# Kernel optimization log

Measured on AMD Instinct MI355X. Metric: run time of the kernel, lower is better.

Reference implementation:

```python
import jax, jax.numpy as jnp
import numpy as np

B, L, DQ, DK, NH = 32, 2048, 1024, 1024, 16
DH = DK // NH  # per-head dim = 64

def setup_inputs() -> dict:
    key = jax.random.key(0)
    ks = jax.random.split(key, 8)
    sq = np.sqrt(2.0 / (DQ + DH)).astype(np.float32)
    sk = np.sqrt(2.0 / (DK + DH)).astype(np.float32)
    return {
        "q": jax.random.normal(ks[0], (B, DQ), jnp.float32),
        "k": jax.random.normal(ks[1], (B, L, DK), jnp.float32),
        "Wq": jax.random.normal(ks[2], (NH * DH, DQ), jnp.float32) * sq,
        "bq": jnp.zeros((NH * DH,), jnp.float32),
        "Wk": jax.random.normal(ks[3], (NH * DH, DK), jnp.float32) * sk,
        "bk": jnp.zeros((NH * DH,), jnp.float32),
        "Wv": jax.random.normal(ks[4], (NH * DH, DK), jnp.float32) * sk,
        "bv": jnp.zeros((NH * DH,), jnp.float32),
    }

def reference(q, k, Wq, bq, Wk, bk, Wv, bv):
    # projections (standard GEMMs), reshape to heads
    qs = (q @ Wq.T + bq).reshape(B, NH, DH)            # [b,n,dh]
    ksr = (k @ Wk.T + bk).reshape(B, L, NH, DH)        # [b,l,n,dh]
    vs = (k @ Wv.T + bv).reshape(B, L, NH, DH)         # [b,l,n,dh]
    temp = jnp.sqrt(jnp.asarray(DH, qs.dtype))
    # single-query attention scores per head, softmax over l
    attn = jnp.einsum('bnd,blnd->bnl', qs, ksr) / temp  # [b,n,l]
    attn = jax.nn.softmax(attn, axis=-1)
    out = jnp.einsum('bnl,blnd->bnd', attn, vs).reshape(B, NH * DH)
    # original returns attn flattened as (n_head*b, l) with head-major order
    attn_flat = jnp.transpose(attn, (1, 0, 2)).reshape(NH * B, L)
    return out, attn_flat
```

## Files before the change

### kernel.cpp

```cpp
#include <hip/hip_runtime.h>
#include <hip/hip_bf16.h>

#define NB 32
#define NL 2048
#define ND 1024
#define NHH 16
#define NDH 64

typedef __bf16 bf16;
typedef __attribute__((ext_vector_type(4))) __bf16 bf16x4;
typedef __attribute__((ext_vector_type(8))) __bf16 bf16x8;
typedef __attribute__((ext_vector_type(4))) float f32x4;

#define SBAR __builtin_amdgcn_s_barrier()
#define WAIT_LGKM0 asm volatile("s_waitcnt lgkmcnt(0)" ::: "memory")
#define WAIT_VM0 asm volatile("s_waitcnt vmcnt(0)" ::: "memory")

#define SWZ(r) (((r) & 7) << 4)

__device__ __forceinline__ float dot4(float4 a, float4 b) {
  return a.x * b.x + a.y * b.y + a.z * b.z + a.w * b.w;
}

__global__ __launch_bounds__(256) void qs_kernel(
    const float* __restrict__ q, const float* __restrict__ Wq,
    const float* __restrict__ bq, float* __restrict__ qs) {
  int o = blockIdx.x;
  int lane = threadIdx.x & 63;
  int wv = threadIdx.x >> 6;
  const float4* wrow = reinterpret_cast<const float4*>(Wq + (size_t)o * ND) + lane * 4;
  float4 w0 = wrow[0], w1 = wrow[1], w2 = wrow[2], w3 = wrow[3];
#pragma unroll
  for (int bb = 0; bb < 8; ++bb) {
    int b = wv * 8 + bb;
    const float4* qr = reinterpret_cast<const float4*>(q + (size_t)b * ND) + lane * 4;
    float s = dot4(qr[0], w0) + dot4(qr[1], w1) + dot4(qr[2], w2) + dot4(qr[3], w3);
#pragma unroll
    for (int off = 32; off > 0; off >>= 1) s += __shfl_down(s, off, 64);
    if (lane == 0) qs[(size_t)b * ND + o] = s + bq[o];
  }
}

__global__ __launch_bounds__(256) void qt_kernel(
    const float* __restrict__ Wk, const float* __restrict__ qs,
    float* __restrict__ qt, const float* __restrict__ bk,
    float* __restrict__ qb) {
  if (blockIdx.x >= 256) {
    int t = (blockIdx.x - 256) * 256 + threadIdx.x;
    if (t < 512) {
      int b = t >> 4, n = t & 15;
      float s = 0.f;
      for (int d = 0; d < 64; ++d)
        s += qs[(size_t)b * ND + n * NDH + d] * bk[n * NDH + d];
      qb[t] = s;
    }
    return;
  }
  int n  = blockIdx.x >> 4;
  int ic = (blockIdx.x >> 2) & 3;
  int bg = blockIdx.x & 3;
  int i = ic * 256 + threadIdx.x;
  __shared__ float s_qs[8][64];
  for (int t = threadIdx.x; t < 512; t += 256) {
    int b = t >> 6, d = t & 63;
    s_qs[b][d] = qs[(size_t)(bg * 8 + b) * ND + n * NDH + d];
  }
  __syncthreads();
  float acc[8];
#pragma unroll
  for (int b = 0; b < 8; ++b) acc[b] = 0.f;
  for (int d = 0; d < 64; ++d) {
    float w = Wk[((size_t)(n * NDH + d)) * ND + i];
#pragma unroll
    for (int b = 0; b < 8; ++b) acc[b] += w * s_qs[b][d];
  }
#pragma unroll
  for (int b = 0; b < 8; ++b)
    qt[((size_t)((bg * 8 + b) * NHH + n)) * ND + i] = acc[b];
}

__global__ __launch_bounds__(512, 4) void fused_kernel(
    const float* __restrict__ kin, const float* __restrict__ qt,
    const float* __restrict__ qb, float* __restrict__ attn,
    float* __restrict__ ctxp) {
  int bx = blockIdx.x;
  int b  = bx >> 3;
  int sl = bx & 7;
  int tid = threadIdx.x, lane = tid & 63, wv = tid >> 6;
  int kg = lane >> 4, ln16 = lane & 15;

  __shared__ __align__(16) float kbf[4][8][1024];
  __shared__ __align__(16) float pbuf[2][8][8][20];
  __shared__ __align__(16) float sP[2][8][20];
  __shared__ __align__(16) float abuf[32][8][16];

  bf16x8 afrag[4];
  {
    const float* qrow = qt + ((size_t)(b * NHH + ln16)) * ND + wv * 128 + kg * 8;
#pragma unroll
    for (int mm = 0; mm < 4; ++mm) {
      f32x4 f0 = *reinterpret_cast<const f32x4*>(qrow + mm * 32);
      f32x4 f1 = *reinterpret_cast<const f32x4*>(qrow + mm * 32 + 4);
      bf16x8 v;
      v[0] = (bf16)f0[0]; v[1] = (bf16)f0[1]; v[2] = (bf16)f0[2]; v[3] = (bf16)f0[3];
      v[4] = (bf16)f1[0]; v[5] = (bf16)f1[1]; v[6] = (bf16)f1[2]; v[7] = (bf16)f1[3];
      afrag[mm] = v;
    }
  }

  int rl = tid & 7, rn = tid >> 3;
  float qbv = (tid < 128) ? qb[b * NHH + rn] : 0.f;

  int nh = tid >> 8, ic = tid & 255;
  f32x4 ctxa[8];
#pragma unroll
  for (int r = 0; r < 8; ++r) ctxa[r] = (f32x4){0.f, 0.f, 0.f, 0.f};

  int sw = SWZ(wv);
  const char* krow0 =
      (const char*)(kin + ((size_t)(b * NL + sl * 256 + wv)) * ND);

#define DMA_TILE(TT, BB)                                                    \
  {                                                                         \
    const char* gsrc = krow0 + (size_t)(TT) * 8 * 4096;                     \
    char* ldst = (char*)kbf + (BB) * 32768 + wv * 4096;                     \
    _Pragma("unroll")                                                       \
    for (int j = 0; j < 4; ++j) {                                           \
      int gb = (j * 1024 + lane * 16) ^ sw;                                 \
      __builtin_amdgcn_global_load_lds(                                     \
          (const unsigned int*)(gsrc + gb),                                 \
          (unsigned int*)(ldst + j * 1024), 16, 0, 0);                      \
    }                                                                       \
  }

  DMA_TILE(0, 0)

  for (int t = -1; t <= 32; ++t) {
    WAIT_VM0;
    WAIT_LGKM0;
    SBAR;

    if (t + 2 <= 31) DMA_TILE(t + 2, (t + 2) & 3)

    if (t + 1 <= 31) {
      const char* kbc = (const char*)kbf + ((t + 1) & 3) * 32768;
      int arow = ln16 & 7;
      int swA = SWZ(arow);
      const char* rb = kbc + arow * 4096;
      f32x4 acc = {0.f, 0.f, 0.f, 0.f};
#pragma unroll
      for (int mm = 0; mm < 4; ++mm) {
        int kcb = (wv * 128 + mm * 32 + kg * 8) * 4;
        f32x4 f0 = *reinterpret_cast<const f32x4*>(rb + (kcb ^ swA));
        f32x4 f1 = *reinterpret_cast<const f32x4*>(rb + (kcb ^ swA ^ 16));
        bf16x8 bfr;
        bfr[0] = (bf16)f0[0]; bfr[1] = (bf16)f0[1];
        bfr[2] = (bf16)f0[2]; bfr[3] = (bf16)f0[3];
        bfr[4] = (bf16)f1[0]; bfr[5] = (bf16)f1[1];
        bfr[6] = (bf16)f1[2]; bfr[7] = (bf16)f1[3];
        acc = __builtin_amdgcn_mfma_f32_16x16x32_bf16(afrag[mm], bfr, acc, 0, 0, 0);
      }
      if (ln16 < 8)
        *reinterpret_cast<f32x4*>(&pbuf[(t + 1) & 1][wv][ln16][kg * 4]) = acc;
    }

    if (t >= 0 && t <= 31 && tid < 128) {
      float s = 0.f;
#pragma unroll
      for (int w = 0; w < 8; ++w) s += pbuf[t & 1][w][rl][rn];
      float p = __expf((s + qbv) * 0.125f);
      sP[t & 1][rl][rn] = p;
      abuf[t][rl][rn] = p;
    }

    if (t >= 1) {
      const char* kbc = (const char*)kbf + ((t - 1) & 3) * 32768;
      const float* sp = &sP[(t - 1) & 1][0][0];
#pragma unroll
      for (int l = 0; l < 8; ++l) {
        const char* rb = kbc + l * 4096;
        f32x4 kf = *reinterpret_cast<const f32x4*>(rb + ((ic * 16) ^ SWZ(l)));
        f32x4 p0 = *reinterpret_cast<const f32x4*>(sp + l * 20 + nh * 8);
        f32x4 p1 = *reinterpret_cast<const f32x4*>(sp + l * 20 + nh * 8 + 4);
#pragma unroll
        for (int n = 0; n < 4; ++n) {
          ctxa[n]     += p0[n] * kf;
          ctxa[4 + n] += p1[n] * kf;
        }
      }
    }
  }
#undef DMA_TILE

#pragma unroll
  for (int n = 0; n < 8; ++n) {
    float* dst = ctxp + (((size_t)sl * NB + b) * NHH + nh * 8 + n) * ND + ic * 4;
    *reinterpret_cast<f32x4*>(dst) = ctxa[n];
  }

  for (int idx = tid; idx < 4096; idx += 512) {
    int n = idx >> 8;
    int ll = idx & 255;
    attn[((size_t)(n * NB + b)) * NL + sl * 256 + ll] = abuf[ll >> 3][ll & 7][n];
  }
}

__global__ __launch_bounds__(256) void normreduce_kernel(
    float* __restrict__ attn, float* __restrict__ invS,
    const float* __restrict__ ctxp, float* __restrict__ ctx) {
  if (blockIdx.x >= 512) {
    size_t e4 = ((size_t)(blockIdx.x - 512) * 256 + threadIdx.x) * 4;
    f32x4 s = *reinterpret_cast<const f32x4*>(ctxp + e4);
#pragma unroll
    for (int sl = 1; sl < 8; ++sl)
      s += *reinterpret_cast<const f32x4*>(ctxp + (size_t)sl * NB * NHH * ND + e4);
    *reinterpret_cast<f32x4*>(ctx + e4) = s;
    return;
  }
  int row = blockIdx.x;
  float* p = attn + (size_t)row * NL;
  int tid = threadIdx.x;
  int lane = tid & 63, wv = tid >> 6;
  float v[8];
  float s = 0.f;
#pragma unroll
  for (int j = 0; j < 8; ++j) {
    v[j] = p[tid + j * 256];
    s += v[j];
  }
#pragma unroll
  for (int off = 32; off > 0; off >>= 1) s += __shfl_down(s, off, 64);
  __shared__ float ss[4];
  if (lane == 0) ss[wv] = s;
  __syncthreads();
  float inv = 1.f / (ss[0] + ss[1] + ss[2] + ss[3]);
  if (tid == 0) invS[row] = inv;
#pragma unroll
  for (int j = 0; j < 8; ++j) p[tid + j * 256] = v[j] * inv;
}

__global__ __launch_bounds__(256) void out_kernel(
    const float* __restrict__ Wv, const float* __restrict__ bv,
    const float* __restrict__ ctx, const float* __restrict__ invS,
    float* __restrict__ out) {
  int o = blockIdx.x;
  int n = o >> 6;
  int lane = threadIdx.x & 63;
  int wv = threadIdx.x >> 6;
  const float4* wrow = reinterpret_cast<const float4*>(Wv + (size_t)o * ND) + lane * 4;
  float4 w0 = wrow[0], w1 = wrow[1], w2 = wrow[2], w3 = wrow[3];
#pragma unroll
  for (int bb = 0; bb < 8; ++bb) {
    int b = wv * 8 + bb;
    const float4* cr =
        reinterpret_cast<const float4*>(ctx + ((size_t)(b * NHH + n)) * ND) + lane * 4;
    float s = dot4(cr[0], w0) + dot4(cr[1], w1) + dot4(cr[2], w2) + dot4(cr[3], w3);
#pragma unroll
    for (int off = 32; off > 0; off >>= 1) s += __shfl_down(s, off, 64);
    if (lane == 0) out[(size_t)b * ND + o] = s * invS[n * NB + b] + bv[o];
  }
}

extern "C" void kernel_launch(void* const* d_in, const int* in_sizes, int n_in,
                              void* d_out, int out_size, void* d_ws, size_t ws_size,
                              hipStream_t stream) {
  const float* q  = (const float*)d_in[0];
  const float* k  = (const float*)d_in[1];
  const float* Wq = (const float*)d_in[2];
  const float* bq = (const float*)d_in[3];
  const float* Wk = (const float*)d_in[4];
  const float* bk = (const float*)d_in[5];
  const float* Wv = (const float*)d_in[6];
  const float* bv = (const float*)d_in[7];

  float* out  = (float*)d_out;
  float* attn = out + NB * ND;

  float* ws   = (float*)d_ws;
  float* qs   = ws;
  float* qt   = ws + 32768;
  float* qb   = qt + 524288;
  float* invS = qb + 512;
  float* ctx  = invS + 512;
  float* ctxp = ctx + 524288;

  qs_kernel<<<1024, 256, 0, stream>>>(q, Wq, bq, qs);
  qt_kernel<<<258, 256, 0, stream>>>(Wk, qs, qt, bk, qb);
  fused_kernel<<<256, 512, 0, stream>>>(k, qt, qb, attn, ctxp);
  normreduce_kernel<<<1024, 256, 0, stream>>>(attn, invS, ctxp, ctx);
  out_kernel<<<1024, 256, 0, stream>>>(Wv, bv, ctx, invS, out);
}
```

Before: 95.40 us.

## Stage K tiles as bf16 via register prefetch and double the L-split

Replaces the direct global-to-LDS DMA of fp32 K tiles with register-staged loads that convert to bf16 before writing to LDS. This halves LDS footprint and read bandwidth and removes the per-use fp32-to-bf16 conversion in the score MFMA path. The grid doubles to 16 L-slices per batch for more parallelism, and the context-partial reduction now sums 16 slices. The risk is extra reduction traffic, bf16 rounding of K in the context accumulation and of the stored attention probabilities, and loss of the asynchronous DMA overlap.

```diff
diff --git a/kernel.cpp b/kernel.cpp
--- a/kernel.cpp
+++ b/kernel.cpp
@@ -14,7 +14,6 @@
 
 #define SBAR __builtin_amdgcn_s_barrier()
 #define WAIT_LGKM0 asm volatile("s_waitcnt lgkmcnt(0)" ::: "memory")
-#define WAIT_VM0 asm volatile("s_waitcnt vmcnt(0)" ::: "memory")
 
 #define SWZ(r) (((r) & 7) << 4)
 
@@ -84,15 +83,15 @@
     const float* __restrict__ qb, float* __restrict__ attn,
     float* __restrict__ ctxp) {
   int bx = blockIdx.x;
-  int b  = bx >> 3;
-  int sl = bx & 7;
+  int b  = bx >> 4;
+  int sl = bx & 15;
   int tid = threadIdx.x, lane = tid & 63, wv = tid >> 6;
   int kg = lane >> 4, ln16 = lane & 15;
 
-  __shared__ __align__(16) float kbf[4][8][1024];
+  __shared__ __align__(16) char  kbf[4][8 * 2048];
   __shared__ __align__(16) float pbuf[2][8][8][20];
   __shared__ __align__(16) float sP[2][8][20];
-  __shared__ __align__(16) float abuf[32][8][16];
+  __shared__ __align__(16) bf16  abuf[16][8][16];
 
   bf16x8 afrag[4];
   {
@@ -111,97 +110,117 @@
   int rl = tid & 7, rn = tid >> 3;
   float qbv = (tid < 128) ? qb[b * NHH + rn] : 0.f;
 
-  int nh = tid >> 8, ic = tid & 255;
+  int nb = tid >> 7, ig = tid & 127;
   f32x4 ctxa[8];
 #pragma unroll
   for (int r = 0; r < 8; ++r) ctxa[r] = (f32x4){0.f, 0.f, 0.f, 0.f};
 
-  int sw = SWZ(wv);
-  const char* krow0 =
-      (const char*)(kin + ((size_t)(b * NL + sl * 256 + wv)) * ND);
-
-#define DMA_TILE(TT, BB)                                                    \
+  int srow = tid >> 7, scol = tid & 127;
+  const float* kblk = kin + ((size_t)(b * NL + sl * 128)) * ND;
+
+#define STAGE_LOAD(TT)                                                      \
   {                                                                         \
-    const char* gsrc = krow0 + (size_t)(TT) * 8 * 4096;                     \
-    char* ldst = (char*)kbf + (BB) * 32768 + wv * 4096;                     \
-    _Pragma("unroll")                                                       \
-    for (int j = 0; j < 4; ++j) {                                           \
-      int gb = (j * 1024 + lane * 16) ^ sw;                                 \
-      __builtin_amdgcn_global_load_lds(                                     \
-          (const unsigned int*)(gsrc + gb),                                 \
-          (unsigned int*)(ldst + j * 1024), 16, 0, 0);                      \
-    }                                                                       \
-  }
-
-  DMA_TILE(0, 0)
-
-  for (int t = -1; t <= 32; ++t) {
-    WAIT_VM0;
+    const float* src = kblk + (size_t)(TT) * 8 * ND;                        \
+    const float* p0 = src + (size_t)srow * ND + scol * 8;                   \
+    s0 = *reinterpret_cast<const f32x4*>(p0);                               \
+    s1 = *reinterpret_cast<const f32x4*>(p0 + 4);                           \
+    const float* p1 = src + (size_t)(srow + 4) * ND + scol * 8;             \
+    s2 = *reinterpret_cast<const f32x4*>(p1);                               \
+    s3 = *reinterpret_cast<const f32x4*>(p1 + 4);                           \
+  }
+
+#define STAGE_WRITE(TT)                                                     \
+  {                                                                         \
+    char* dst = kbf[(TT) & 3];                                              \
+    bf16x8 v0, v1;                                                          \
+    v0[0] = (bf16)s0[0]; v0[1] = (bf16)s0[1];                               \
+    v0[2] = (bf16)s0[2]; v0[3] = (bf16)s0[3];                               \
+    v0[4] = (bf16)s1[0]; v0[5] = (bf16)s1[1];                               \
+    v0[6] = (bf16)s1[2]; v0[7] = (bf16)s1[3];                               \
+    v1[0] = (bf16)s2[0]; v1[1] = (bf16)s2[1];                               \
+    v1[2] = (bf16)s2[2]; v1[3] = (bf16)s2[3];                               \
+    v1[4] = (bf16)s3[0]; v1[5] = (bf16)s3[1];                               \
+    v1[6] = (bf16)s3[2]; v1[7] = (bf16)s3[3];                               \
+    *reinterpret_cast<bf16x8*>(dst + srow * 2048 +                          \
+                               ((scol * 16) ^ SWZ(srow))) = v0;             \
+    *reinterpret_cast<bf16x8*>(dst + (srow + 4) * 2048 +                    \
+                               ((scol * 16) ^ SWZ(srow + 4))) = v1;         \
+  }
+
+  f32x4 s0, s1, s2, s3;
+
+  STAGE_LOAD(0)
+  STAGE_WRITE(0)
+
+  for (int t = -1; t <= 16; ++t) {
     WAIT_LGKM0;
     SBAR;
 
-    if (t + 2 <= 31) DMA_TILE(t + 2, (t + 2) & 3)
-
-    if (t + 1 <= 31) {
-      const char* kbc = (const char*)kbf + ((t + 1) & 3) * 32768;
+    if (t + 2 <= 15) STAGE_LOAD(t + 2)
+
+    if (t + 1 <= 15) {
+      const char* kbc = kbf[(t + 1) & 3];
       int arow = ln16 & 7;
       int swA = SWZ(arow);
-      const char* rb = kbc + arow * 4096;
+      const char* rb = kbc + arow * 2048;
       f32x4 acc = {0.f, 0.f, 0.f, 0.f};
 #pragma unroll
       for (int mm = 0; mm < 4; ++mm) {
-        int kcb = (wv * 128 + mm * 32 + kg * 8) * 4;
-        f32x4 f0 = *reinterpret_cast<const f32x4*>(rb + (kcb ^ swA));
-        f32x4 f1 = *reinterpret_cast<const f32x4*>(rb + (kcb ^ swA ^ 16));
-        bf16x8 bfr;
-        bfr[0] = (bf16)f0[0]; bfr[1] = (bf16)f0[1];
-        bfr[2] = (bf16)f0[2]; bfr[3] = (bf16)f0[3];
-        bfr[4] = (bf16)f1[0]; bfr[5] = (bf16)f1[1];
-        bfr[6] = (bf16)f1[2]; bfr[7] = (bf16)f1[3];
+        int kcb2 = (wv * 128 + mm * 32 + kg * 8) * 2;
+        bf16x8 bfr = *reinterpret_cast<const bf16x8*>(rb + (kcb2 ^ swA));
         acc = __builtin_amdgcn_mfma_f32_16x16x32_bf16(afrag[mm], bfr, acc, 0, 0, 0);
       }
       if (ln16 < 8)
         *reinterpret_cast<f32x4*>(&pbuf[(t + 1) & 1][wv][ln16][kg * 4]) = acc;
     }
 
-    if (t >= 0 && t <= 31 && tid < 128) {
+    if (t >= 0 && t <= 15 && tid < 128) {
       float s = 0.f;
 #pragma unroll
       for (int w = 0; w < 8; ++w) s += pbuf[t & 1][w][rl][rn];
       float p = __expf((s + qbv) * 0.125f);
       sP[t & 1][rl][rn] = p;
-      abuf[t][rl][rn] = p;
+      abuf[t][rl][rn] = (bf16)p;
     }
 
     if (t >= 1) {
-      const char* kbc = (const char*)kbf + ((t - 1) & 3) * 32768;
+      const char* kbc = kbf[(t - 1) & 3];
       const float* sp = &sP[(t - 1) & 1][0][0];
 #pragma unroll
       for (int l = 0; l < 8; ++l) {
-        const char* rb = kbc + l * 4096;
-        f32x4 kf = *reinterpret_cast<const f32x4*>(rb + ((ic * 16) ^ SWZ(l)));
-        f32x4 p0 = *reinterpret_cast<const f32x4*>(sp + l * 20 + nh * 8);
-        f32x4 p1 = *reinterpret_cast<const f32x4*>(sp + l * 20 + nh * 8 + 4);
+        bf16x8 kv = *reinterpret_cast<const bf16x8*>(
+            kbc + l * 2048 + ((ig * 16) ^ SWZ(l)));
+        f32x4 pv = *reinterpret_cast<const f32x4*>(sp + l * 20 + nb * 4);
+        f32x4 k0, k1;
+        k0[0] = (float)kv[0]; k0[1] = (float)kv[1];
+        k0[2] = (float)kv[2]; k0[3] = (float)kv[3];
+        k1[0] = (float)kv[4]; k1[1] = (float)kv[5];
+        k1[2] = (float)kv[6]; k1[3] = (float)kv[7];
 #pragma unroll
         for (int n = 0; n < 4; ++n) {
-          ctxa[n]     += p0[n] * kf;
-          ctxa[4 + n] += p1[n] * kf;
+          ctxa[n * 2]     += pv[n] * k0;
+          ctxa[n * 2 + 1] += pv[n] * k1;
         }
       }
     }
-  }
-#undef DMA_TILE
-
-#pragma unroll
-  for (int n = 0; n < 8; ++n) {
-    float* dst = ctxp + (((size_t)sl * NB + b) * NHH + nh * 8 + n) * ND + ic * 4;
-    *reinterpret_cast<f32x4*>(dst) = ctxa[n];
-  }
-
-  for (int idx = tid; idx < 4096; idx += 512) {
-    int n = idx >> 8;
-    int ll = idx & 255;
-    attn[((size_t)(n * NB + b)) * NL + sl * 256 + ll] = abuf[ll >> 3][ll & 7][n];
+
+    if (t + 2 <= 15) STAGE_WRITE(t + 2)
+  }
+#undef STAGE_LOAD
+#undef STAGE_WRITE
+
+#pragma unroll
+  for (int n = 0; n < 4; ++n) {
+    float* dst = ctxp + (((size_t)sl * NB + b) * NHH + nb * 4 + n) * ND + ig * 8;
+    *reinterpret_cast<f32x4*>(dst)     = ctxa[n * 2];
+    *reinterpret_cast<f32x4*>(dst + 4) = ctxa[n * 2 + 1];
+  }
+
+  for (int idx = tid; idx < 2048; idx += 512) {
+    int n = idx >> 7;
+    int ll = idx & 127;
+    attn[((size_t)(n * NB + b)) * NL + sl * 128 + ll] =
+        (float)abuf[ll >> 3][ll & 7][n];
   }
 }
 
@@ -212,7 +231,7 @@
     size_t e4 = ((size_t)(blockIdx.x - 512) * 256 + threadIdx.x) * 4;
     f32x4 s = *reinterpret_cast<const f32x4*>(ctxp + e4);
 #pragma unroll
-    for (int sl = 1; sl < 8; ++sl)
+    for (int sl = 1; sl < 16; ++sl)
       s += *reinterpret_cast<const f32x4*>(ctxp + (size_t)sl * NB * NHH * ND + e4);
     *reinterpret_cast<f32x4*>(ctx + e4) = s;
     return;
@@ -286,7 +305,7 @@
 
   qs_kernel<<<1024, 256, 0, stream>>>(q, Wq, bq, qs);
   qt_kernel<<<258, 256, 0, stream>>>(Wk, qs, qt, bk, qb);
-  fused_kernel<<<256, 512, 0, stream>>>(k, qt, qb, attn, ctxp);
+  fused_kernel<<<512, 512, 0, stream>>>(k, qt, qb, attn, ctxp);
   normreduce_kernel<<<1024, 256, 0, stream>>>(attn, invS, ctxp, ctx);
   out_kernel<<<1024, 256, 0, stream>>>(Wv, bv, ctx, invS, out);
 }
```

After: 175.2 us. 1.84x slower.
